# Kernel tuning notes

Hardware: AMD Instinct MI355X
Metric: run time of the kernel (lower is better)

The kernel has to match this reference:

```python
import jax, jax.numpy as jnp
import numpy as np

N_NODES = 50000
N_EDGES = 1600000
D = 64            # gin_hidden_units == embedding_dim
N_GRAPHS = 512
N_CLASSES = 53
ITERS = 3
VOCAB = 3100
BN_EPS = 1e-5


def setup_inputs() -> dict:
    key = jax.random.key(0)
    ks = jax.random.split(key, 16)
    pkt_length = jax.random.randint(ks[0], (N_NODES,), 0, VOCAB, dtype=jnp.int32)
    src = jax.random.randint(ks[1], (N_EDGES,), 0, N_NODES, dtype=jnp.int32)
    dst = jax.random.randint(ks[2], (N_EDGES,), 0, N_NODES, dtype=jnp.int32)
    graph_ids = jnp.sort(jax.random.randint(ks[3], (N_NODES,), 0, N_GRAPHS, dtype=jnp.int32))
    s = 0.05
    emb = jax.random.normal(ks[4], (VOCAB, D), dtype=jnp.float32) * s
    eps = jnp.zeros((), dtype=jnp.float32)  # GINConv learn_eps init 0
    W1 = jax.random.normal(ks[5], (D, D), dtype=jnp.float32) * s
    b1 = jnp.zeros((D,), dtype=jnp.float32)
    W2 = jax.random.normal(ks[6], (D, D), dtype=jnp.float32) * s
    b2 = jnp.zeros((D,), dtype=jnp.float32)
    W3 = jax.random.normal(ks[7], (D, D), dtype=jnp.float32) * s
    b3 = jnp.zeros((D,), dtype=jnp.float32)
    gamma = jnp.ones((D,), dtype=jnp.float32)
    beta = jnp.zeros((D,), dtype=jnp.float32)
    Wc = jax.random.normal(ks[8], (ITERS * D, N_CLASSES), dtype=jnp.float32) * s
    bc = jnp.zeros((N_CLASSES,), dtype=jnp.float32)
    return {"pkt_length": pkt_length, "src": src, "dst": dst, "graph_ids": graph_ids,
            "emb": emb, "eps": eps, "W1": W1, "b1": b1, "W2": W2, "b2": b2,
            "W3": W3, "b3": b3, "gamma": gamma, "beta": beta, "Wc": Wc, "bc": bc}


def _mlp_bn(x, W1, b1, W2, b2, W3, b3, gamma, beta):
    # 3 Linear+ReLU layers, then BatchNorm1d (training-mode batch stats)
    x = jax.nn.relu(x @ W1 + b1)
    x = jax.nn.relu(x @ W2 + b2)
    x = jax.nn.relu(x @ W3 + b3)
    mean = jnp.mean(x, axis=0)
    var = jnp.var(x, axis=0)
    return gamma * (x - mean) * jax.lax.rsqrt(var + BN_EPS) + beta


def reference(pkt_length, src, dst, graph_ids, emb, eps, W1, b1, W2, b2, W3, b3, gamma, beta, Wc, bc):
    # node features via embedding lookup
    h = emb[pkt_length]  # [N, D]
    pooled = []
    for _ in range(ITERS):
        # GIN sum aggregation: agg[v] = sum_{(u->v)} h[u]
        agg = jax.ops.segment_sum(h[src], dst, num_segments=N_NODES)
        h = _mlp_bn((1.0 + eps) * h + agg, W1, b1, W2, b2, W3, b3, gamma, beta)
        # graph sum pooling
        pooled.append(jax.ops.segment_sum(h, graph_ids, num_segments=N_GRAPHS))
    graph_features = jnp.concatenate(pooled, axis=-1)  # [G, 3*D]
    return graph_features @ Wc + bc  # [G, nb_classes]
```

## Files before the change

kernel.cpp:

```cpp
#include <hip/hip_runtime.h>

#define N_NODES   50000
#define N_EDGES   1600000
#define DDIM      64
#define N_GRAPHS  512
#define N_CLASSES 53
#define ITERS     3
#define NB        782
#define NBLK      391
#define PPITCH    400
#define NPB       128
#define CHUNK     ((N_EDGES + NPB - 1) / NPB)
#define NZERO     (NB + N_GRAPHS)

typedef __bf16 bf16x8 __attribute__((ext_vector_type(8)));
typedef __bf16 bf16x4 __attribute__((ext_vector_type(4)));
typedef float  f32x4  __attribute__((ext_vector_type(4)));

__device__ __forceinline__ float blo16(unsigned w) { return __uint_as_float(w << 16); }
__device__ __forceinline__ float bhi16(unsigned w) { return __uint_as_float(w & 0xffff0000u); }

__global__ void embed_kernel(const int* __restrict__ pkt, const float4* __restrict__ emb,
                             bf16x4* __restrict__ hb4, int* __restrict__ zreg) {
  if (blockIdx.x == 0) {
    for (int i = threadIdx.x; i < NZERO; i += 256) zreg[i] = 0;
  }
  int idx = blockIdx.x * 256 + threadIdx.x;
  if (idx >= N_NODES * 16) return;
  int node = idx >> 4;
  float4 v = emb[(size_t)pkt[node] * 16 + (idx & 15)];
  bf16x4 o;
  o[0] = (__bf16)v.x; o[1] = (__bf16)v.y; o[2] = (__bf16)v.z; o[3] = (__bf16)v.w;
  hb4[idx] = o;
}

__global__ void bucket_hist_kernel(const int* __restrict__ dst, int* __restrict__ bhist) {
  __shared__ int lh[NB];
  for (int i = threadIdx.x; i < NB; i += 256) lh[i] = 0;
  __syncthreads();
  int stride = gridDim.x * 256;
  for (int e = blockIdx.x * 256 + threadIdx.x; e < N_EDGES; e += stride)
    atomicAdd(&lh[dst[e] >> 6], 1);
  __syncthreads();
  for (int i = threadIdx.x; i < NB; i += 256)
    if (lh[i]) atomicAdd(&bhist[i], lh[i]);
}

__global__ void hist_kernel(const int* __restrict__ idx, int* __restrict__ counts, int n) {
  int i = blockIdx.x * 256 + threadIdx.x;
  if (i < n) atomicAdd(&counts[idx[i]], 1);
}

__device__ void scan_body(const int* __restrict__ counts, int* __restrict__ offs,
                          int* __restrict__ cursor, int n) {
  __shared__ int wsum[16];
  __shared__ int carry;
  int tid = threadIdx.x;
  if (tid == 0) carry = 0;
  __syncthreads();
  for (int base = 0; base < n; base += 1024) {
    int i = base + tid;
    int v = (i < n) ? counts[i] : 0;
    int x = v;
    #pragma unroll
    for (int off = 1; off < 64; off <<= 1) {
      int y = __shfl_up(x, off);
      if ((tid & 63) >= off) x += y;
    }
    int w = tid >> 6;
    if ((tid & 63) == 63) wsum[w] = x;
    __syncthreads();
    int woff = 0;
    for (int k = 0; k < w; ++k) woff += wsum[k];
    int incl = x + woff + carry;
    if (i < n) {
      offs[i] = incl - v;
      if (cursor) cursor[i] = incl - v;
    }
    __syncthreads();
    if (tid == 1023) carry = incl;
    __syncthreads();
  }
  if (tid == 0) offs[n] = carry;
}

__global__ void scans_kernel(const int* __restrict__ bhist, int* __restrict__ boffs,
                             int* __restrict__ bcursor, const int* __restrict__ gcnt,
                             int* __restrict__ goff) {
  if (blockIdx.x == 0) scan_body(bhist, boffs, bcursor, NB);
  else                 scan_body(gcnt, goff, nullptr, N_GRAPHS);
}

__global__ __launch_bounds__(1024) void partition_kernel(
    const int* __restrict__ src, const int* __restrict__ dst,
    int* __restrict__ bcursor, unsigned* __restrict__ ebuf) {
  __shared__ int lh[NB];
  __shared__ int lbase[NB];
  for (int i = threadIdx.x; i < NB; i += 1024) lh[i] = 0;
  __syncthreads();
  int e0 = blockIdx.x * CHUNK;
  int e1 = min(e0 + CHUNK, N_EDGES);
  for (int e = e0 + (int)threadIdx.x; e < e1; e += 1024)
    atomicAdd(&lh[dst[e] >> 6], 1);
  __syncthreads();
  for (int i = threadIdx.x; i < NB; i += 1024) {
    int c = lh[i];
    lbase[i] = c ? atomicAdd(&bcursor[i], c) : 0;
    lh[i] = 0;
  }
  __syncthreads();
  for (int e = e0 + (int)threadIdx.x; e < e1; e += 1024) {
    int d = dst[e];
    int b = d >> 6;
    int pos = lbase[b] + atomicAdd(&lh[b], 1);
    ebuf[pos] = (unsigned)src[e] | ((unsigned)(d & 63) << 16);
  }
}

__global__ __launch_bounds__(256) void local_scatter_kernel(
    const unsigned* __restrict__ ebuf, const int* __restrict__ boffs,
    int* __restrict__ offs, int* __restrict__ csr) {
  __shared__ int cnt[64];
  __shared__ int base[64];
  const int b = blockIdx.x;
  const int tid = threadIdx.x;
  if (tid < 64) cnt[tid] = 0;
  __syncthreads();
  const int ebeg = boffs[b], eend = boffs[b + 1];
  for (int e = ebeg + tid; e < eend; e += 256)
    atomicAdd(&cnt[(ebuf[e] >> 16) & 63u], 1);
  __syncthreads();
  if (tid < 64) {
    int v = cnt[tid];
    int x = v;
    #pragma unroll
    for (int off = 1; off < 64; off <<= 1) {
      int y = __shfl_up(x, off);
      if (tid >= off) x += y;
    }
    int excl = ebeg + x - v;
    base[tid] = excl;
    int node = b * 64 + tid;
    if (node < N_NODES) offs[node] = excl;
    cnt[tid] = 0;
  }
  __syncthreads();
  for (int e = ebeg + tid; e < eend; e += 256) {
    unsigned p = ebuf[e];
    int j = (p >> 16) & 63u;
    int pos = base[j] + atomicAdd(&cnt[j], 1);
    csr[pos] = (int)(p & 0xFFFFu);
  }
  if (b == NB - 1 && tid == 0) offs[N_NODES] = N_EDGES;
}

__global__ void pack_weights_kernel(const float* __restrict__ W1, const float* __restrict__ W2,
                                    const float* __restrict__ W3, bf16x8* __restrict__ wbuf) {
  int i = blockIdx.x * 256 + threadIdx.x;
  if (i >= 24 * 64) return;
  int lane = i & 63;
  int frag = i >> 6;
  int t = frag & 3;
  int kc = (frag >> 2) & 1;
  int L = frag >> 3;
  const float* W = (L == 0) ? W1 : ((L == 1) ? W2 : W3);
  int l15 = lane & 15, lg = lane >> 4;
  bf16x8 fh, fl;
  #pragma unroll
  for (int e = 0; e < 8; ++e) {
    int k = kc * 32 + lg * 8 + e;
    float w = W[k * 64 + t * 16 + l15];
    __bf16 hi = (__bf16)w;
    fh[e] = hi;
    fl[e] = (__bf16)(w - (float)hi);
  }
  wbuf[i] = fh;
  wbuf[24 * 64 + i] = fl;
}

__device__ __forceinline__ void split8(const f32x4& v0, const f32x4& v1,
                                       bf16x8& hi, bf16x8& lo) {
  #pragma unroll
  for (int e = 0; e < 4; ++e) {
    __bf16 h0 = (__bf16)v0[e];
    __bf16 h1 = (__bf16)v1[e];
    hi[e] = h0;     lo[e] = (__bf16)(v0[e] - (float)h0);
    hi[4 + e] = h1; lo[4 + e] = (__bf16)(v1[e] - (float)h1);
  }
}

#define MFMA(A, B, C) __builtin_amdgcn_mfma_f32_16x16x32_bf16((A), (B), (C), 0, 0, 0)

#define DOT(L, T, BIASV, ACC)                                        \
  {                                                                  \
    bf16x8 bh0 = wbuf[(((L) * 2 + 0) * 4 + (T)) * 64 + lane];        \
    bf16x8 bh1 = wbuf[(((L) * 2 + 1) * 4 + (T)) * 64 + lane];        \
    bf16x8 bl0 = wbuf[1536 + (((L) * 2 + 0) * 4 + (T)) * 64 + lane]; \
    bf16x8 bl1 = wbuf[1536 + (((L) * 2 + 1) * 4 + (T)) * 64 + lane]; \
    f32x4 a_ = {(BIASV), (BIASV), (BIASV), (BIASV)};                 \
    a_ = MFMA(A0h, bh0, a_);                                         \
    a_ = MFMA(A1h, bh1, a_);                                         \
    a_ = MFMA(A0l, bh0, a_);                                         \
    a_ = MFMA(A1l, bh1, a_);                                         \
    a_ = MFMA(A0h, bl0, a_);                                         \
    a_ = MFMA(A1h, bl1, a_);                                         \
    ACC = a_;                                                        \
  }

#define DOLAYER(L)                   \
  DOT(L, 0, bias##L[0], acc0)        \
  DOT(L, 1, bias##L[1], acc1)        \
  DOT(L, 2, bias##L[2], acc2)        \
  DOT(L, 3, bias##L[3], acc3)

#define STORE_T(T, A)                                         \
  sc[(4 * lg + 0) * 68 + (T) * 16 + l15] = fmaxf(A[0], 0.f);  \
  sc[(4 * lg + 1) * 68 + (T) * 16 + l15] = fmaxf(A[1], 0.f);  \
  sc[(4 * lg + 2) * 68 + (T) * 16 + l15] = fmaxf(A[2], 0.f);  \
  sc[(4 * lg + 3) * 68 + (T) * 16 + l15] = fmaxf(A[3], 0.f);

#define TRANSITION                                            \
  {                                                           \
    STORE_T(0, acc0)                                          \
    STORE_T(1, acc1)                                          \
    STORE_T(2, acc2)                                          \
    STORE_T(3, acc3)                                          \
    const float* rp = sc + l15 * 68 + lg * 8;                 \
    f32x4 r0 = *(const f32x4*)(rp);                           \
    f32x4 r1 = *(const f32x4*)(rp + 4);                       \
    f32x4 r2 = *(const f32x4*)(rp + 32);                      \
    f32x4 r3 = *(const f32x4*)(rp + 36);                      \
    split8(r0, r1, A0h, A0l);                                 \
    split8(r2, r3, A1h, A1l);                                 \
  }

#define EPI_T(T, A)                                                       \
  {                                                                       \
    float v0 = fmaxf(A[0], 0.f), v1 = fmaxf(A[1], 0.f);                   \
    float v2 = fmaxf(A[2], 0.f), v3 = fmaxf(A[3], 0.f);                   \
    if (active) {                                                         \
      xout[(size_t)(rows0 + 4 * lg + 0) * DDIM + (T) * 16 + l15] = v0;    \
      xout[(size_t)(rows0 + 4 * lg + 1) * DDIM + (T) * 16 + l15] = v1;    \
      xout[(size_t)(rows0 + 4 * lg + 2) * DDIM + (T) * 16 + l15] = v2;    \
      xout[(size_t)(rows0 + 4 * lg + 3) * DDIM + (T) * 16 + l15] = v3;    \
    }                                                                     \
    float vs = (v0 + v1) + (v2 + v3);                                     \
    float vq = ((v0 * v0 + v1 * v1) + (v2 * v2 + v3 * v3));               \
    vs += __shfl_xor(vs, 16); vs += __shfl_xor(vs, 32);                   \
    vq += __shfl_xor(vq, 16); vq += __shfl_xor(vq, 32);                   \
    if (lane < 16) {                                                      \
      bnred[0][wave][(T) * 16 + l15] = vs;                                \
      bnred[1][wave][(T) * 16 + l15] = vq;                                \
    }                                                                     \
  }

__global__ __launch_bounds__(512) void agg_mlp_kernel(
    const __bf16* __restrict__ hb, const int* __restrict__ offs,
    const int* __restrict__ csr, const float* __restrict__ epsp,
    float* __restrict__ xout, const bf16x8* __restrict__ wbuf,
    const float* __restrict__ b1, const float* __restrict__ b2,
    const float* __restrict__ b3, float* __restrict__ partial) {
  __shared__ float xt[8 * 16 * 68];
  __shared__ float bnred[2][8][64];
  const int tid = threadIdx.x;
  const int lane = tid & 63, wave = tid >> 6;
  const int l15 = lane & 15, lg = lane >> 4;
  const int rows0 = blockIdx.x * 128 + wave * 16;
  const bool active = rows0 < N_NODES;
  float* xw = xt + wave * (16 * 68);

  {
    const int fl = lane & 7, eg = lane >> 3;
    const uint4* __restrict__ hrow4 = (const uint4*)hb;
    const float ep = 1.0f + epsp[0];
    #pragma unroll
    for (int pass = 0; pass < 2; ++pass) {
      const int node = rows0 + pass * 8 + eg;
      int beg = 0, end = 0;
      if (active) { beg = offs[node]; end = offs[node + 1]; }
      const int deg = end - beg;
      int maxdeg = deg;
      maxdeg = max(maxdeg, __shfl_xor(maxdeg, 8));
      maxdeg = max(maxdeg, __shfl_xor(maxdeg, 16));
      maxdeg = max(maxdeg, __shfl_xor(maxdeg, 32));

      float a0 = 0.f, a1 = 0.f, a2 = 0.f, a3 = 0.f,
            a4 = 0.f, a5 = 0.f, a6 = 0.f, a7 = 0.f;
      if (active) {
        uint4 w = hrow4[(size_t)node * 8 + fl];
        a0 = ep * blo16(w.x); a1 = ep * bhi16(w.x);
        a2 = ep * blo16(w.y); a3 = ep * bhi16(w.y);
        a4 = ep * blo16(w.z); a5 = ep * bhi16(w.z);
        a6 = ep * blo16(w.w); a7 = ep * bhi16(w.w);
      }
      #pragma unroll 4
      for (int it = 0; it < maxdeg; ++it) {
        bool act = it < deg;
        int ci = beg + it;
        ci = (ci < N_EDGES) ? ci : 0;
        int u = csr[ci];
        uint4 w = hrow4[(size_t)u * 8 + fl];
        unsigned m = act ? 0xffffffffu : 0u;
        w.x &= m; w.y &= m; w.z &= m; w.w &= m;
        a0 += blo16(w.x); a1 += bhi16(w.x);
        a2 += blo16(w.y); a3 += bhi16(w.y);
        a4 += blo16(w.z); a5 += bhi16(w.z);
        a6 += blo16(w.w); a7 += bhi16(w.w);
      }
      float* xp = xw + (pass * 8 + eg) * 68 + fl * 8;
      float4 o0 = {a0, a1, a2, a3};
      float4 o1 = {a4, a5, a6, a7};
      *(float4*)xp = o0;
      *(float4*)(xp + 4) = o1;
    }
  }

  f32x4 acc0 = {0.f, 0.f, 0.f, 0.f}, acc1 = acc0, acc2 = acc0, acc3 = acc0;
  if (active) {
    float bias0[4], bias1[4], bias2[4];
    #pragma unroll
    for (int t = 0; t < 4; ++t) {
      bias0[t] = b1[t * 16 + l15];
      bias1[t] = b2[t * 16 + l15];
      bias2[t] = b3[t * 16 + l15];
    }
    float* sc = xw;
    bf16x8 A0h, A0l, A1h, A1l;
    {
      const float* rp = xw + l15 * 68 + lg * 8;
      f32x4 r0 = *(const f32x4*)(rp);
      f32x4 r1 = *(const f32x4*)(rp + 4);
      f32x4 r2 = *(const f32x4*)(rp + 32);
      f32x4 r3 = *(const f32x4*)(rp + 36);
      split8(r0, r1, A0h, A0l);
      split8(r2, r3, A1h, A1l);
    }
    DOLAYER(0)
    TRANSITION
    DOLAYER(1)
    TRANSITION
    DOLAYER(2)
  }

  EPI_T(0, acc0)
  EPI_T(1, acc1)
  EPI_T(2, acc2)
  EPI_T(3, acc3)

  __syncthreads();
  if (tid < 128) {
    int s = tid >> 6, c = tid & 63;
    float t = 0.f;
    #pragma unroll
    for (int w = 0; w < 8; ++w) t += bnred[s][w][c];
    partial[(size_t)tid * PPITCH + blockIdx.x] = t;
  }
}

__global__ void bn_stats_kernel(const float* __restrict__ partial,
                                float* __restrict__ colsum) {
  int row = blockIdx.x * 4 + (threadIdx.x >> 6);
  int lane = threadIdx.x & 63;
  const float* rp = partial + (size_t)row * PPITCH;
  float acc = 0.f;
  for (int i = lane; i < NBLK; i += 64) acc += rp[i];
  #pragma unroll
  for (int off = 32; off > 0; off >>= 1) acc += __shfl_down(acc, off);
  if (lane == 0) colsum[row] = acc;
}

__global__ void norm_pool_kernel(const float* __restrict__ x, __bf16* __restrict__ hb,
                                 float* __restrict__ pooled, const int* __restrict__ goff,
                                 const float* __restrict__ colsum, const float* __restrict__ gamma,
                                 const float* __restrict__ beta, int iter) {
  int g = blockIdx.x;
  int lane = threadIdx.x & 63;
  int wave = threadIdx.x >> 6;
  const float invN = 1.0f / N_NODES;
  float mean = colsum[lane] * invN;
  float var = colsum[64 + lane] * invN - mean * mean;
  float inv = 1.0f / sqrtf(var + 1e-5f);
  float gm = gamma[lane] * inv;
  float bt = beta[lane] - mean * gm;
  int rbeg = goff[g], rend = goff[g + 1];
  float acc = 0.f;
  for (int r = rbeg + wave; r < rend; r += 4) {
    float v = fmaf(x[(size_t)r * DDIM + lane], gm, bt);
    hb[(size_t)r * DDIM + lane] = (__bf16)v;
    acc += v;
  }
  __shared__ float red[4][64];
  red[wave][lane] = acc;
  __syncthreads();
  if (wave == 0) {
    pooled[(size_t)g * (ITERS * DDIM) + iter * DDIM + lane] =
        red[0][lane] + red[1][lane] + red[2][lane] + red[3][lane];
  }
}

__global__ void classifier_kernel(const float* __restrict__ pooled, const float* __restrict__ Wc,
                                  const float* __restrict__ bc, float* __restrict__ out) {
  int g = blockIdx.x;
  int c = threadIdx.x;
  if (c >= N_CLASSES) return;
  float acc = bc[c];
  #pragma unroll 4
  for (int k = 0; k < ITERS * DDIM; ++k)
    acc = fmaf(pooled[(size_t)g * (ITERS * DDIM) + k], Wc[k * N_CLASSES + c], acc);
  out[(size_t)g * N_CLASSES + c] = acc;
}

extern "C" void kernel_launch(void* const* d_in, const int* in_sizes, int n_in,
                              void* d_out, int out_size, void* d_ws, size_t ws_size,
                              hipStream_t stream) {
  const int*   pkt   = (const int*)d_in[0];
  const int*   src   = (const int*)d_in[1];
  const int*   dst   = (const int*)d_in[2];
  const int*   gids  = (const int*)d_in[3];
  const float* emb   = (const float*)d_in[4];
  const float* eps   = (const float*)d_in[5];
  const float* W1    = (const float*)d_in[6];
  const float* b1    = (const float*)d_in[7];
  const float* W2    = (const float*)d_in[8];
  const float* b2    = (const float*)d_in[9];
  const float* W3    = (const float*)d_in[10];
  const float* b3    = (const float*)d_in[11];
  const float* gamma = (const float*)d_in[12];
  const float* beta  = (const float*)d_in[13];
  const float* Wc    = (const float*)d_in[14];
  const float* bc    = (const float*)d_in[15];
  float* out = (float*)d_out;

  char* p = (char*)d_ws;
  auto alloc = [&](size_t bytes) {
    char* r = p;
    p += (bytes + 255) & ~(size_t)255;
    return r;
  };
  __bf16*   hb      = (__bf16*)alloc((size_t)N_NODES * DDIM * 2);
  float*    x       = (float*)alloc((size_t)N_NODES * DDIM * 4);
  unsigned* ebuf    = (unsigned*)alloc((size_t)N_EDGES * 4);
  int*      csr     = (int*)alloc((size_t)N_EDGES * 4);
  int*      offs    = (int*)alloc((size_t)(N_NODES + 1) * 4);
  int*      boffs   = (int*)alloc((size_t)(NB + 1) * 4);
  int*      bcursor = (int*)alloc((size_t)NB * 4);
  int*      goff    = (int*)alloc((size_t)(N_GRAPHS + 1) * 4);
  float*    pooled  = (float*)alloc((size_t)N_GRAPHS * ITERS * DDIM * 4);
  float*    colsum  = (float*)alloc(128 * 4);
  bf16x8*   wbuf    = (bf16x8*)alloc((size_t)48 * 64 * 16);
  float*    partial = (float*)alloc((size_t)128 * PPITCH * 4);
  int*   zreg  = (int*)alloc((size_t)NZERO * 4);
  int*   bhist = zreg;
  int*   gcnt  = bhist + NB;

  embed_kernel<<<(N_NODES * 16 + 255) / 256, 256, 0, stream>>>(pkt, (const float4*)emb,
                                                               (bf16x4*)hb, zreg);
  bucket_hist_kernel<<<512, 256, 0, stream>>>(dst, bhist);
  hist_kernel<<<(N_NODES + 255) / 256, 256, 0, stream>>>(gids, gcnt, N_NODES);
  scans_kernel<<<2, 1024, 0, stream>>>(bhist, boffs, bcursor, gcnt, goff);
  partition_kernel<<<NPB, 1024, 0, stream>>>(src, dst, bcursor, ebuf);
  local_scatter_kernel<<<NB, 256, 0, stream>>>(ebuf, boffs, offs, csr);
  pack_weights_kernel<<<6, 256, 0, stream>>>(W1, W2, W3, wbuf);

  for (int it = 0; it < ITERS; ++it) {
    agg_mlp_kernel<<<NBLK, 512, 0, stream>>>(hb, offs, csr, eps, x, wbuf,
                                             b1, b2, b3, partial);
    bn_stats_kernel<<<32, 256, 0, stream>>>(partial, colsum);
    norm_pool_kernel<<<N_GRAPHS, 256, 0, stream>>>(x, hb, pooled, goff, colsum, gamma, beta, it);
  }
  classifier_kernel<<<N_GRAPHS, 64, 0, stream>>>(pooled, Wc, bc, out);
}
```

Baseline: 266.5 us.

## Fold BatchNorm affine into next aggregation and store pre-norm activations as bf16

The BN normalization is no longer applied in a separate pass that rewrites h. Instead the raw ReLU output is stored as bf16, and the next iteration's aggregation applies gamma/beta algebraically as gm*sum + (1+eps+deg)*bt. Pooling likewise applies the affine to per-graph sums using the row count. This removes the fp32 x write/read and the bf16 rewrite of h each iteration, at the cost of rounding the pre-norm values to bf16 and slightly different numerics.

```diff
diff --git a/kernel.cpp b/kernel.cpp
--- a/kernel.cpp
+++ b/kernel.cpp
@@ -21,9 +21,11 @@
 __device__ __forceinline__ float bhi16(unsigned w) { return __uint_as_float(w & 0xffff0000u); }
 
 __global__ void embed_kernel(const int* __restrict__ pkt, const float4* __restrict__ emb,
-                             bf16x4* __restrict__ hb4, int* __restrict__ zreg) {
+                             bf16x4* __restrict__ hb4, int* __restrict__ zreg,
+                             float* __restrict__ gmbt_id) {
   if (blockIdx.x == 0) {
     for (int i = threadIdx.x; i < NZERO; i += 256) zreg[i] = 0;
+    if (threadIdx.x < 128) gmbt_id[threadIdx.x] = (threadIdx.x < 64) ? 1.0f : 0.0f;
   }
   int idx = blockIdx.x * 256 + threadIdx.x;
   if (idx >= N_NODES * 16) return;
@@ -234,30 +236,31 @@
     split8(r2, r3, A1h, A1l);                                 \
   }
 
-#define EPI_T(T, A)                                                       \
-  {                                                                       \
-    float v0 = fmaxf(A[0], 0.f), v1 = fmaxf(A[1], 0.f);                   \
-    float v2 = fmaxf(A[2], 0.f), v3 = fmaxf(A[3], 0.f);                   \
-    if (active) {                                                         \
-      xout[(size_t)(rows0 + 4 * lg + 0) * DDIM + (T) * 16 + l15] = v0;    \
-      xout[(size_t)(rows0 + 4 * lg + 1) * DDIM + (T) * 16 + l15] = v1;    \
-      xout[(size_t)(rows0 + 4 * lg + 2) * DDIM + (T) * 16 + l15] = v2;    \
-      xout[(size_t)(rows0 + 4 * lg + 3) * DDIM + (T) * 16 + l15] = v3;    \
-    }                                                                     \
-    float vs = (v0 + v1) + (v2 + v3);                                     \
-    float vq = ((v0 * v0 + v1 * v1) + (v2 * v2 + v3 * v3));               \
-    vs += __shfl_xor(vs, 16); vs += __shfl_xor(vs, 32);                   \
-    vq += __shfl_xor(vq, 16); vq += __shfl_xor(vq, 32);                   \
-    if (lane < 16) {                                                      \
-      bnred[0][wave][(T) * 16 + l15] = vs;                                \
-      bnred[1][wave][(T) * 16 + l15] = vq;                                \
-    }                                                                     \
+#define EPI_T(T, A)                                                         \
+  {                                                                         \
+    float v0 = fmaxf(A[0], 0.f), v1 = fmaxf(A[1], 0.f);                     \
+    float v2 = fmaxf(A[2], 0.f), v3 = fmaxf(A[3], 0.f);                     \
+    if (active) {                                                           \
+      xbout[(size_t)(rows0 + 4 * lg + 0) * DDIM + (T) * 16 + l15] = (__bf16)v0; \
+      xbout[(size_t)(rows0 + 4 * lg + 1) * DDIM + (T) * 16 + l15] = (__bf16)v1; \
+      xbout[(size_t)(rows0 + 4 * lg + 2) * DDIM + (T) * 16 + l15] = (__bf16)v2; \
+      xbout[(size_t)(rows0 + 4 * lg + 3) * DDIM + (T) * 16 + l15] = (__bf16)v3; \
+    }                                                                       \
+    float vs = (v0 + v1) + (v2 + v3);                                       \
+    float vq = ((v0 * v0 + v1 * v1) + (v2 * v2 + v3 * v3));                 \
+    vs += __shfl_xor(vs, 16); vs += __shfl_xor(vs, 32);                     \
+    vq += __shfl_xor(vq, 16); vq += __shfl_xor(vq, 32);                     \
+    if (lane < 16) {                                                        \
+      bnred[0][wave][(T) * 16 + l15] = vs;                                  \
+      bnred[1][wave][(T) * 16 + l15] = vq;                                  \
+    }                                                                       \
   }
 
 __global__ __launch_bounds__(512) void agg_mlp_kernel(
-    const __bf16* __restrict__ hb, const int* __restrict__ offs,
+    const __bf16* __restrict__ xbin, const int* __restrict__ offs,
     const int* __restrict__ csr, const float* __restrict__ epsp,
-    float* __restrict__ xout, const bf16x8* __restrict__ wbuf,
+    const float* __restrict__ gmbt, __bf16* __restrict__ xbout,
+    const bf16x8* __restrict__ wbuf,
     const float* __restrict__ b1, const float* __restrict__ b2,
     const float* __restrict__ b3, float* __restrict__ partial) {
   __shared__ float xt[8 * 16 * 68];
@@ -271,8 +274,12 @@
 
   {
     const int fl = lane & 7, eg = lane >> 3;
-    const uint4* __restrict__ hrow4 = (const uint4*)hb;
+    const uint4* __restrict__ hrow4 = (const uint4*)xbin;
     const float ep = 1.0f + epsp[0];
+    f32x4 gA = *(const f32x4*)(gmbt + fl * 8);
+    f32x4 gB = *(const f32x4*)(gmbt + fl * 8 + 4);
+    f32x4 tA = *(const f32x4*)(gmbt + 64 + fl * 8);
+    f32x4 tB = *(const f32x4*)(gmbt + 64 + fl * 8 + 4);
     #pragma unroll
     for (int pass = 0; pass < 2; ++pass) {
       const int node = rows0 + pass * 8 + eg;
@@ -307,6 +314,11 @@
         a4 += blo16(w.z); a5 += bhi16(w.z);
         a6 += blo16(w.w); a7 += bhi16(w.w);
       }
+      const float fdeg = ep + (float)deg;
+      a0 = fmaf(gA[0], a0, fdeg * tA[0]); a1 = fmaf(gA[1], a1, fdeg * tA[1]);
+      a2 = fmaf(gA[2], a2, fdeg * tA[2]); a3 = fmaf(gA[3], a3, fdeg * tA[3]);
+      a4 = fmaf(gB[0], a4, fdeg * tB[0]); a5 = fmaf(gB[1], a5, fdeg * tB[1]);
+      a6 = fmaf(gB[2], a6, fdeg * tB[2]); a7 = fmaf(gB[3], a7, fdeg * tB[3]);
       float* xp = xw + (pass * 8 + eg) * 68 + fl * 8;
       float4 o0 = {a0, a1, a2, a3};
       float4 o1 = {a4, a5, a6, a7};
@@ -358,43 +370,55 @@
 }
 
 __global__ void bn_stats_kernel(const float* __restrict__ partial,
-                                float* __restrict__ colsum) {
-  int row = blockIdx.x * 4 + (threadIdx.x >> 6);
+                                const float* __restrict__ gamma,
+                                const float* __restrict__ beta,
+                                float* __restrict__ gmbt) {
+  int d = blockIdx.x * 4 + (threadIdx.x >> 6);
   int lane = threadIdx.x & 63;
-  const float* rp = partial + (size_t)row * PPITCH;
-  float acc = 0.f;
-  for (int i = lane; i < NBLK; i += 64) acc += rp[i];
+  const float* rs = partial + (size_t)d * PPITCH;
+  const float* rq = partial + (size_t)(64 + d) * PPITCH;
+  float s = 0.f, q = 0.f;
+  for (int i = lane; i < NBLK; i += 64) { s += rs[i]; q += rq[i]; }
   #pragma unroll
-  for (int off = 32; off > 0; off >>= 1) acc += __shfl_down(acc, off);
-  if (lane == 0) colsum[row] = acc;
-}
-
-__global__ void norm_pool_kernel(const float* __restrict__ x, __bf16* __restrict__ hb,
-                                 float* __restrict__ pooled, const int* __restrict__ goff,
-                                 const float* __restrict__ colsum, const float* __restrict__ gamma,
-                                 const float* __restrict__ beta, int iter) {
-  int g = blockIdx.x;
-  int lane = threadIdx.x & 63;
-  int wave = threadIdx.x >> 6;
-  const float invN = 1.0f / N_NODES;
-  float mean = colsum[lane] * invN;
-  float var = colsum[64 + lane] * invN - mean * mean;
-  float inv = 1.0f / sqrtf(var + 1e-5f);
-  float gm = gamma[lane] * inv;
-  float bt = beta[lane] - mean * gm;
-  int rbeg = goff[g], rend = goff[g + 1];
-  float acc = 0.f;
-  for (int r = rbeg + wave; r < rend; r += 4) {
-    float v = fmaf(x[(size_t)r * DDIM + lane], gm, bt);
-    hb[(size_t)r * DDIM + lane] = (__bf16)v;
-    acc += v;
-  }
-  __shared__ float red[4][64];
-  red[wave][lane] = acc;
-  __syncthreads();
-  if (wave == 0) {
-    pooled[(size_t)g * (ITERS * DDIM) + iter * DDIM + lane] =
-        red[0][lane] + red[1][lane] + red[2][lane] + red[3][lane];
+  for (int off = 32; off > 0; off >>= 1) {
+    s += __shfl_down(s, off);
+    q += __shfl_down(q, off);
+  }
+  if (lane == 0) {
+    const float invN = 1.0f / N_NODES;
+    float mean = s * invN;
+    float var = q * invN - mean * mean;
+    float gm = gamma[d] / sqrtf(var + 1e-5f);
+    gmbt[d] = gm;
+    gmbt[64 + d] = beta[d] - mean * gm;
+  }
+}
+
+__global__ void pool_kernel(const unsigned* __restrict__ xbu, const int* __restrict__ goff,
+                            const float* __restrict__ gmbt, float* __restrict__ pooled,
+                            int iter) {
+  const int g = blockIdx.x;
+  const int tid = threadIdx.x;
+  const int c = tid & 31;
+  const int slot = tid >> 5;
+  const int rbeg = goff[g], rend = goff[g + 1];
+  float a0 = 0.f, a1 = 0.f;
+  for (int r = rbeg + slot; r < rend; r += 8) {
+    unsigned w = xbu[(size_t)r * 32 + c];
+    a0 += blo16(w);
+    a1 += bhi16(w);
+  }
+  __shared__ float red[8][64];
+  red[slot][2 * c] = a0;
+  red[slot][2 * c + 1] = a1;
+  __syncthreads();
+  if (tid < 64) {
+    float s = 0.f;
+    #pragma unroll
+    for (int k = 0; k < 8; ++k) s += red[k][tid];
+    float cnt = (float)(rend - rbeg);
+    pooled[(size_t)g * (ITERS * DDIM) + iter * DDIM + tid] =
+        fmaf(gmbt[tid], s, cnt * gmbt[64 + tid]);
   }
 }
 
@@ -438,7 +462,8 @@
     return r;
   };
   __bf16*   hb      = (__bf16*)alloc((size_t)N_NODES * DDIM * 2);
-  float*    x       = (float*)alloc((size_t)N_NODES * DDIM * 4);
+  __bf16*   xb0     = (__bf16*)alloc((size_t)N_NODES * DDIM * 2);
+  __bf16*   xb1     = (__bf16*)alloc((size_t)N_NODES * DDIM * 2);
   unsigned* ebuf    = (unsigned*)alloc((size_t)N_EDGES * 4);
   int*      csr     = (int*)alloc((size_t)N_EDGES * 4);
   int*      offs    = (int*)alloc((size_t)(N_NODES + 1) * 4);
@@ -446,15 +471,16 @@
   int*      bcursor = (int*)alloc((size_t)NB * 4);
   int*      goff    = (int*)alloc((size_t)(N_GRAPHS + 1) * 4);
   float*    pooled  = (float*)alloc((size_t)N_GRAPHS * ITERS * DDIM * 4);
-  float*    colsum  = (float*)alloc(128 * 4);
+  float*    gmbt    = (float*)alloc(128 * 4);
+  float*    gmbt_id = (float*)alloc(128 * 4);
   bf16x8*   wbuf    = (bf16x8*)alloc((size_t)48 * 64 * 16);
   float*    partial = (float*)alloc((size_t)128 * PPITCH * 4);
   int*   zreg  = (int*)alloc((size_t)NZERO * 4);
   int*   bhist = zreg;
   int*   gcnt  = bhist + NB;
 
-  embed_kernel<<<(N_NODES * 16 + 255) / 256, 256, 0, stream>>>(pkt, (const float4*)emb,
-                                                               (bf16x4*)hb, zreg);
+  embed_kernel<<<(N_NODES * 16 + 255) / 256, 256, 0, stream>>>(
+      pkt, (const float4*)emb, (bf16x4*)hb, zreg, gmbt_id);
   bucket_hist_kernel<<<512, 256, 0, stream>>>(dst, bhist);
   hist_kernel<<<(N_NODES + 255) / 256, 256, 0, stream>>>(gids, gcnt, N_NODES);
   scans_kernel<<<2, 1024, 0, stream>>>(bhist, boffs, bcursor, gcnt, goff);
@@ -462,11 +488,15 @@
   local_scatter_kernel<<<NB, 256, 0, stream>>>(ebuf, boffs, offs, csr);
   pack_weights_kernel<<<6, 256, 0, stream>>>(W1, W2, W3, wbuf);
 
+  const __bf16* xin[ITERS]  = {hb, xb0, xb1};
+  __bf16*       xout[ITERS] = {xb0, xb1, xb0};
   for (int it = 0; it < ITERS; ++it) {
-    agg_mlp_kernel<<<NBLK, 512, 0, stream>>>(hb, offs, csr, eps, x, wbuf,
-                                             b1, b2, b3, partial);
-    bn_stats_kernel<<<32, 256, 0, stream>>>(partial, colsum);
-    norm_pool_kernel<<<N_GRAPHS, 256, 0, stream>>>(x, hb, pooled, goff, colsum, gamma, beta, it);
+    const float* aff = (it == 0) ? gmbt_id : gmbt;
+    agg_mlp_kernel<<<NBLK, 512, 0, stream>>>(xin[it], offs, csr, eps, aff,
+                                             xout[it], wbuf, b1, b2, b3, partial);
+    bn_stats_kernel<<<16, 256, 0, stream>>>(partial, gamma, beta, gmbt);
+    pool_kernel<<<N_GRAPHS, 256, 0, stream>>>((const unsigned*)xout[it], goff,
+                                              gmbt, pooled, it);
   }
   classifier_kernel<<<N_GRAPHS, 64, 0, stream>>>(pooled, Wc, bc, out);
 }
```

After: 241.2 us, median of 2. -9.5%, faster.
